# Performance work log

Hardware: AMD Instinct MI355X
Metric: run time of the kernel (lower is better)

## Reference

```python
import jax, jax.numpy as jnp
import numpy as np

B, D, E = 8, 256, 2048
H, DK, DV = 8, 32, 32
LN_EPS = 1e-6
MASK_FILL = -1e9


def setup_inputs() -> dict:
    key = jax.random.key(0)
    ks = jax.random.split(key, 6)
    scale = 1.0 / np.sqrt(D)
    x = jax.random.normal(ks[0], (B, D, E), dtype=jnp.float32)
    mask = jax.random.randint(ks[1], (B, E, E), 0, 2).astype(bool)
    w_qs = jax.random.normal(ks[2], (D, H * DK), dtype=jnp.float32) * scale
    w_ks = jax.random.normal(ks[3], (D, H * DK), dtype=jnp.float32) * scale
    w_vs = jax.random.normal(ks[4], (D, H * DV), dtype=jnp.float32) * scale
    w_fc = jax.random.normal(ks[5], (H * DV, D), dtype=jnp.float32) * scale
    ln_gamma = jnp.ones((D,), dtype=jnp.float32)
    ln_beta = jnp.zeros((D,), dtype=jnp.float32)
    return {"x": x, "mask": mask, "w_qs": w_qs, "w_ks": w_ks,
            "w_vs": w_vs, "w_fc": w_fc, "ln_gamma": ln_gamma, "ln_beta": ln_beta}


def reference(x, mask, w_qs, w_ks, w_vs, w_fc, ln_gamma, ln_beta):
    # x: [B, D, E] -> s: [B, E, D]  (edges as sequence, features as d_model)
    s = jnp.transpose(x, (0, 2, 1))
    residual = s
    # LayerNorm applied to queries only (as in the original MultiHeadAttention)
    mu = jnp.mean(s, axis=-1, keepdims=True)
    var = jnp.mean((s - mu) ** 2, axis=-1, keepdims=True)
    q_in = (s - mu) * jax.lax.rsqrt(var + LN_EPS) * ln_gamma + ln_beta
    # projections -> [B, H, E, dk/dv]
    q = (q_in @ w_qs).reshape(B, E, H, DK).transpose(0, 2, 1, 3)
    k = (s @ w_ks).reshape(B, E, H, DK).transpose(0, 2, 1, 3)
    v = (s @ w_vs).reshape(B, E, H, DV).transpose(0, 2, 1, 3)
    temperature = jnp.sqrt(jnp.asarray(DK, dtype=q.dtype))
    scores = jnp.einsum('bhqd,bhkd->bhqk', q / temperature, k)
    scores = jnp.where(mask[:, None, :, :], scores, MASK_FILL)
    attn = jax.nn.softmax(scores, axis=-1)  # [B, H, E, E]
    out = jnp.einsum('bhqk,bhkd->bhqd', attn, v)
    out = out.transpose(0, 2, 1, 3).reshape(B, E, H * DV)
    out = out @ w_fc + residual  # dropout is identity in eval mode
    x_out = jnp.transpose(out, (0, 2, 1))  # back to [B, D, E]
    # attention-per-edge diagnostic (no gradient in original: attn.detach())
    attn_d = jax.lax.stop_gradient(attn)
    m = mask[:, None, :, :].astype(attn.dtype)  # [B, 1, E, E]
    attn_per_edge = jnp.sum(attn_d * m, axis=(1, 2)) / jnp.sum(m, axis=(1, 2))
    return (x_out, attn, attn_per_edge)
```

## Files before the change

### kernel.cpp

```cpp
#include <hip/hip_runtime.h>
#include <hip/hip_fp16.h>
#include <math.h>

#define TB 8
#define TD 256
#define TE 2048
#define TH 8

typedef _Float16 h8 __attribute__((ext_vector_type(8)));
typedef float    f4 __attribute__((ext_vector_type(4)));

static __device__ __forceinline__ unsigned int packh2(float a, float b){
  __half2 h = __floats2half2_rn(a, b);
  return __builtin_bit_cast(unsigned int, h);
}

__global__ __launch_bounds__(256) void k_pack(const unsigned int* __restrict__ mraw,
                       unsigned int* __restrict__ packed, float* __restrict__ num){
  __shared__ int oks;
  const int t = threadIdx.x;
  if(t == 0) oks = 1;
  __syncthreads();
  int ok = 1;
  for(int i=t; i<4096; i+=256) if(mraw[i] > 1u) ok = 0;
  if(!ok) atomicAnd(&oks, 0);
  __syncthreads();
  const int isInt = oks;

  const int row = blockIdx.x*4 + (t >> 6);
  const int w = t & 63;
  const size_t base = (size_t)row*TE + (size_t)w*32;
  unsigned int bits = 0;
  if(isInt){
    const unsigned int* p = mraw + base;
    #pragma unroll
    for(int j=0;j<32;j++) bits |= (p[j] & 1u) << j;
  } else {
    const unsigned char* p = (const unsigned char*)mraw + base;
    #pragma unroll
    for(int j=0;j<32;j++) bits |= (unsigned int)(p[j] != 0) << j;
  }
  packed[(size_t)row*64 + w] = bits;
  if(blockIdx.x < 64) num[blockIdx.x*256 + t] = 0.f;
}

__global__ __launch_bounds__(256) void k_denom(const unsigned int* __restrict__ packed,
                        float* __restrict__ denom){
  const int b = blockIdx.z;
  const int k = blockIdx.x*256 + threadIdx.x;
  const int q0 = blockIdx.y*64;
  const unsigned int* p = packed + ((size_t)b*TE + q0)*64 + (k >> 5);
  const unsigned sh = k & 31;
  int cnt = 0;
  #pragma unroll 8
  for(int q=0;q<64;q++) cnt += (p[(size_t)q*64] >> sh) & 1u;
  atomicAdd(&denom[b*TE + k], (float)cnt);
}

__global__ __launch_bounds__(256) void k_wpack(
    const float* __restrict__ wqs, const float* __restrict__ wks,
    const float* __restrict__ wvs, const float* __restrict__ wfc,
    _Float16* __restrict__ qkvT, _Float16* __restrict__ fcT){
  const int n = blockIdx.x;
  const int k = threadIdx.x;
  if(n < 256)      qkvT[(size_t)n*256 + k] = (_Float16)wqs[(size_t)k*256 + n];
  else if(n < 512) qkvT[(size_t)n*256 + k] = (_Float16)wks[(size_t)k*256 + (n-256)];
  else if(n < 768) qkvT[(size_t)n*256 + k] = (_Float16)wvs[(size_t)k*256 + (n-512)];
  else             fcT[(size_t)(n-768)*256 + k] = (_Float16)wfc[(size_t)k*256 + (n-768)];
}

__global__ __launch_bounds__(256) void k_qkv(
    const float* __restrict__ x, const _Float16* __restrict__ qkvT,
    const float* __restrict__ gamma, const float* __restrict__ beta,
    _Float16* __restrict__ qh, _Float16* __restrict__ kh, _Float16* __restrict__ vt){
  __shared__ float xs[16][260];
  __shared__ __align__(16) _Float16 xh[16][264];
  __shared__ __align__(16) _Float16 qn[16][264];
  __shared__ float mu_s[16], rs_s[16];
  const int t = threadIdx.x;
  const int b = blockIdx.y;
  const int e0 = blockIdx.x*16;

  for(int i=t;i<16*256;i+=256){
    int el = i & 15, dd = i >> 4;
    xs[el][dd] = x[((size_t)(b*TD + dd))*TE + e0 + el];
  }
  __syncthreads();
  {
    int row = t >> 4, j = t & 15;
    float s1=0.f, s2=0.f;
    #pragma unroll
    for(int i=0;i<16;i++){ float v = xs[row][j*16+i]; s1 += v; s2 += v*v; }
    #pragma unroll
    for(int off=1; off<16; off<<=1){ s1 += __shfl_xor(s1, off); s2 += __shfl_xor(s2, off); }
    if(j==0){
      float m = s1 * (1.f/256.f);
      float var = s2 * (1.f/256.f) - m*m;
      mu_s[row] = m;
      rs_s[row] = rsqrtf(var + 1e-6f);
    }
  }
  __syncthreads();
  for(int i=t;i<16*256;i+=256){
    int r = i >> 8, dd = i & 255;
    float xv = xs[r][dd];
    xh[r][dd] = (_Float16)xv;
    qn[r][dd] = (_Float16)((xv - mu_s[r]) * rs_s[r] * gamma[dd] + beta[dd]);
  }
  __syncthreads();

  const int w = t >> 6, l = t & 63, g = l >> 4, c = l & 15;
  const f4 f4z = {0.f,0.f,0.f,0.f};
  const float sclq = 0.17677669529663687f * 1.44269504088896f;
  h8 af[8];

  #pragma unroll
  for(int kk=0;kk<8;kk++) af[kk] = *(const h8*)&qn[c][kk*32 + g*8];
  #pragma unroll
  for(int i=0;i<4;i++){
    const int n0 = (4*w+i)*16;
    f4 acc = f4z;
    #pragma unroll
    for(int kk=0;kk<8;kk++){
      h8 bf = *(const h8*)(qkvT + (size_t)(n0 + c)*256 + kk*32 + g*8);
      acc = __builtin_amdgcn_mfma_f32_16x16x32_f16(bf, af[kk], acc, 0, 0, 0);
    }
    const int d0 = n0 + 4*g, hh = d0 >> 5, d2 = d0 & 31;
    uint2 ov;
    ov.x = packh2(acc[0]*sclq, acc[1]*sclq);
    ov.y = packh2(acc[2]*sclq, acc[3]*sclq);
    *(uint2*)&qh[((size_t)(b*TH+hh)*TE + e0 + c)*32 + d2] = ov;
  }
  #pragma unroll
  for(int kk=0;kk<8;kk++) af[kk] = *(const h8*)&xh[c][kk*32 + g*8];
  #pragma unroll
  for(int i=0;i<4;i++){
    const int n0 = (4*w+i)*16;
    f4 acc = f4z;
    #pragma unroll
    for(int kk=0;kk<8;kk++){
      h8 bf = *(const h8*)(qkvT + (size_t)(256 + n0 + c)*256 + kk*32 + g*8);
      acc = __builtin_amdgcn_mfma_f32_16x16x32_f16(bf, af[kk], acc, 0, 0, 0);
    }
    const int d0 = n0 + 4*g, hh = d0 >> 5, d2 = d0 & 31;
    uint2 ov;
    ov.x = packh2(acc[0], acc[1]);
    ov.y = packh2(acc[2], acc[3]);
    *(uint2*)&kh[((size_t)(b*TH+hh)*TE + e0 + c)*32 + d2] = ov;
  }
  const int jj = (e0 >> 4) & 1;
  const int p = c & 3, a = c >> 2;
  #pragma unroll
  for(int i=0;i<4;i++){
    const int n0 = (4*w+i)*16;
    f4 acc = f4z;
    #pragma unroll
    for(int kk=0;kk<8;kk++){
      h8 bf = *(const h8*)(qkvT + (size_t)(512 + n0 + c)*256 + kk*32 + g*8);
      acc = __builtin_amdgcn_mfma_f32_16x16x32_f16(bf, af[kk], acc, 0, 0, 0);
    }
    f4 n_, fv;
    #pragma unroll
    for(int r=0;r<4;r++){
      float o = __shfl_xor(acc[r^1], 1);
      n_[r] = ((p^r)&1) ? o : acc[r];
    }
    #pragma unroll
    for(int r=0;r<4;r++){
      float o = __shfl_xor(n_[r^2], 2);
      fv[r] = ((p^r)&2) ? o : n_[r];
    }
    const int d = n0 + 4*g + p;
    uint2 ov;
    ov.x = packh2(fv[0], fv[1]);
    ov.y = packh2(fv[2], fv[3]);
    *(uint2*)&vt[((size_t)(b*TH + (d>>5))*32 + (d&31))*TE + (e0 & ~31) + 8*a + 4*jj] = ov;
  }
}

__global__ __launch_bounds__(256) void k_attn(
    const _Float16* __restrict__ qh, const _Float16* __restrict__ kh, const _Float16* __restrict__ vt,
    const unsigned int* __restrict__ packed,
    float* __restrict__ attn, _Float16* __restrict__ owh, float* __restrict__ num){
  __shared__ __align__(16) unsigned int mb[64][66];
  __shared__ float num_s[TE];
  __shared__ __align__(16) f4 S4[4][272];

  const int t = threadIdx.x;
  int bid = blockIdx.x;
  bid = (bid & 7) * 256 + (bid >> 3);
  const int qt = bid & 31;
  const int bhid = bid >> 5;
  const int h = bhid & 7, b = bhid >> 3;
  const size_t bh = (size_t)bhid * TE;
  const _Float16* Qg = qh + bh*32;
  const _Float16* Kg = kh + bh*32;
  const _Float16* Vg = vt + bh*32;
  const int q0 = qt*64;

  const int wid = t >> 6, l = t & 63, g = l >> 4, c = l & 15;
  const int qr = wid*16 + c;
  const f4 f4z = {0.f, 0.f, 0.f, 0.f};

  for(int i=t;i<TE;i+=256) num_s[i] = 0.f;
  for(int i=t;i<64*64;i+=256){
    int r = i >> 6, w = i & 63;
    mb[r][w] = packed[((size_t)b*TE + q0 + r)*64 + w];
  }
  __syncthreads();

  const h8 qf = *(const h8*)(Qg + (size_t)(q0 + qr)*32 + g*8);

  float ll = 0.f;
  for(int kt=0; kt<32; ++kt){
    h8 kf[4];
    #pragma unroll
    for(int j=0;j<4;j++) kf[j] = *(const h8*)(Kg + (size_t)(kt*64 + j*16 + c)*32 + g*8);
    f4 s[4];
    #pragma unroll
    for(int j=0;j<4;j++) s[j] = __builtin_amdgcn_mfma_f32_16x16x32_f16(kf[j], qf, f4z, 0, 0, 0);
    const uint2 mw2 = *(const uint2*)&mb[qr][2*kt];
    #pragma unroll
    for(int j=0;j<4;j++){
      const unsigned mw = (j>>1) ? mw2.y : mw2.x;
      #pragma unroll
      for(int r=0;r<4;r++){
        float sv = ((mw >> ((j&1)*16 + 4*g + r)) & 1u) ? s[j][r] : -1e9f;
        ll += exp2f(sv);
      }
    }
  }
  ll += __shfl_xor(ll, 16);
  ll += __shfl_xor(ll, 32);
  const float rl = 1.f / ll;

  f4 oacc[2] = {f4z, f4z};
  f4* Sw = S4[wid];
  float* abase = attn + (bh + q0 + wid*16)*TE;
  for(int kt=0; kt<32; ++kt){
    h8 kf[4];
    #pragma unroll
    for(int j=0;j<4;j++) kf[j] = *(const h8*)(Kg + (size_t)(kt*64 + j*16 + c)*32 + g*8);
    f4 s[4];
    #pragma unroll
    for(int j=0;j<4;j++) s[j] = __builtin_amdgcn_mfma_f32_16x16x32_f16(kf[j], qf, f4z, 0, 0, 0);
    const uint2 mw2 = *(const uint2*)&mb[qr][2*kt];
    unsigned int pk[4][2];
    #pragma unroll
    for(int j=0;j<4;j++){
      const unsigned mw = (j>>1) ? mw2.y : mw2.x;
      f4 p;
      #pragma unroll
      for(int r=0;r<4;r++){
        float sv = ((mw >> ((j&1)*16 + 4*g + r)) & 1u) ? s[j][r] : -1e9f;
        p[r] = exp2f(sv) * rl;
      }
      Sw[c*17 + 4*j + g] = p;
      pk[j][0] = packh2(p[0], p[1]);
      pk[j][1] = packh2(p[2], p[3]);
    }
    #pragma unroll
    for(int kc=0;kc<2;kc++){
      uint4 pu = {pk[2*kc][0], pk[2*kc][1], pk[2*kc+1][0], pk[2*kc+1][1]};
      h8 pf = __builtin_bit_cast(h8, pu);
      #pragma unroll
      for(int du=0;du<2;du++){
        h8 vf = *(const h8*)(Vg + (size_t)(du*16 + c)*TE + kt*64 + kc*32 + g*8);
        oacc[du] = __builtin_amdgcn_mfma_f32_16x16x32_f16(vf, pf, oacc[du], 0, 0, 0);
      }
    }
    f4 v[4];
    #pragma unroll
    for(int u=0;u<4;u++) v[u] = Sw[(u*4+g)*17 + c];
    #pragma unroll
    for(int u=0;u<4;u++)
      __builtin_nontemporal_store(v[u], (f4*)(abase + (size_t)(u*4+g)*TE + kt*64 + c*4));
    f4 a = v[0] + v[1] + v[2] + v[3];
    #pragma unroll
    for(int q=0;q<4;q++){ a[q] += __shfl_xor(a[q], 16); a[q] += __shfl_xor(a[q], 32); }
    if(l < 16){
      float* np = &num_s[kt*64 + c*4];
      atomicAdd(np+0, a[0]); atomicAdd(np+1, a[1]);
      atomicAdd(np+2, a[2]); atomicAdd(np+3, a[3]);
    }
  }

  #pragma unroll
  for(int du=0;du<2;du++){
    uint2 ov;
    ov.x = packh2(oacc[du][0], oacc[du][1]);
    ov.y = packh2(oacc[du][2], oacc[du][3]);
    *(uint2*)&owh[((size_t)b*TE + q0 + qr)*256 + h*32 + du*16 + 4*g] = ov;
  }
  __syncthreads();
  for(int i=t;i<TE;i+=256) atomicAdd(&num[(size_t)b*TE + i], num_s[i]);
}

__global__ __launch_bounds__(256) void k_fc(
    const _Float16* __restrict__ owh, const _Float16* __restrict__ fcT,
    const float* __restrict__ x, float* __restrict__ xout){
  __shared__ float xt[16][260];
  const int t = threadIdx.x;
  const int b = blockIdx.y;
  const int e0 = blockIdx.x * 16;
  for(int i=t;i<4096;i+=256){
    int el = i & 15, dd = i >> 4;
    xt[el][dd] = x[((size_t)(b*TD + dd))*TE + e0 + el];
  }
  const int w = t >> 6, l = t & 63, g = l >> 4, c = l & 15;
  h8 af[8];
  #pragma unroll
  for(int kk=0;kk<8;kk++)
    af[kk] = *(const h8*)(owh + ((size_t)b*TE + e0 + c)*256 + kk*32 + g*8);
  f4 accs[4];
  #pragma unroll
  for(int i=0;i<4;i++){
    const int n0 = w*64 + i*16;
    f4 acc = {0.f,0.f,0.f,0.f};
    #pragma unroll
    for(int kk=0;kk<8;kk++){
      h8 bf = *(const h8*)(fcT + (size_t)(n0 + c)*256 + kk*32 + g*8);
      acc = __builtin_amdgcn_mfma_f32_16x16x32_f16(bf, af[kk], acc, 0, 0, 0);
    }
    accs[i] = acc;
  }
  __syncthreads();
  #pragma unroll
  for(int i=0;i<4;i++){
    const int n0 = w*64 + i*16 + 4*g;
    #pragma unroll
    for(int r=0;r<4;r++) xt[c][n0+r] += accs[i][r];
  }
  __syncthreads();
  for(int i=t;i<4096;i+=256){
    int el = i & 15, dd = i >> 4;
    xout[((size_t)(b*TD + dd))*TE + e0 + el] = xt[el][dd];
  }
}

__global__ void k_edge(const float* __restrict__ num, const float* __restrict__ denom,
                       float* __restrict__ pe){
  int idx = blockIdx.x*256 + threadIdx.x;
  pe[idx] = num[idx] / (8.f * denom[idx]);
}

extern "C" void kernel_launch(void* const* d_in, const int* in_sizes, int n_in,
                              void* d_out, int out_size, void* d_ws, size_t ws_size,
                              hipStream_t stream){
  const float* x   = (const float*)d_in[0];
  const unsigned int* mraw = (const unsigned int*)d_in[1];
  const float* wqs = (const float*)d_in[2];
  const float* wks = (const float*)d_in[3];
  const float* wvs = (const float*)d_in[4];
  const float* wfc = (const float*)d_in[5];
  const float* gamma = (const float*)d_in[6];
  const float* beta  = (const float*)d_in[7];

  float* xout = (float*)d_out;
  float* attn = xout + (size_t)TB*TD*TE;
  float* pe   = attn + (size_t)TB*TH*TE*TE;

  const size_t SZ = (size_t)TB*TH*TE*32;
  _Float16* qhp = (_Float16*)((char*)d_ws + 256);
  _Float16* khp = qhp + SZ;
  _Float16* vtp = khp + SZ;
  _Float16* owh = vtp + SZ;
  unsigned int* packed = (unsigned int*)(owh + SZ);
  float* num   = (float*)(packed + (size_t)TB*TE*64);
  float* denom = num + (size_t)TB*TE;
  _Float16* qkvT = (_Float16*)(denom + (size_t)TB*TE);
  _Float16* fcT  = qkvT + 768*256;

  hipMemsetAsync(denom, 0, (size_t)TB*TE*sizeof(float), stream);
  k_wpack<<<1024, 256, 0, stream>>>(wqs, wks, wvs, wfc, qkvT, fcT);
  k_pack<<<TB*TE/4, 256, 0, stream>>>(mraw, packed, num);
  k_denom<<<dim3(TE/256, TE/64, TB), 256, 0, stream>>>(packed, denom);
  k_qkv<<<dim3(TE/16, TB), 256, 0, stream>>>(x, qkvT, gamma, beta, qhp, khp, vtp);
  k_attn<<<TB*TH*TE/64, 256, 0, stream>>>(qhp, khp, vtp, packed, attn, owh, num);
  k_fc<<<dim3(TE/16, TB), 256, 0, stream>>>(owh, fcT, x, xout);
  k_edge<<<TB*TE/256, 256, 0, stream>>>(num, denom, pe);
}
```

Before: 403.8 us.

## Fuse mask column counts into coalesced ballot-based mask packing; drop k_denom

```diff
diff --git a/kernel.cpp b/kernel.cpp
--- a/kernel.cpp
+++ b/kernel.cpp
@@ -16,8 +16,10 @@
 }
 
 __global__ __launch_bounds__(256) void k_pack(const unsigned int* __restrict__ mraw,
-                       unsigned int* __restrict__ packed, float* __restrict__ num){
+                       unsigned int* __restrict__ packed, float* __restrict__ denom,
+                       float* __restrict__ num){
   __shared__ int oks;
+  __shared__ unsigned int ps[32][66];
   const int t = threadIdx.x;
   if(t == 0) oks = 1;
   __syncthreads();
@@ -27,34 +29,34 @@
   __syncthreads();
   const int isInt = oks;
 
-  const int row = blockIdx.x*4 + (t >> 6);
-  const int w = t & 63;
-  const size_t base = (size_t)row*TE + (size_t)w*32;
-  unsigned int bits = 0;
-  if(isInt){
-    const unsigned int* p = mraw + base;
-    #pragma unroll
-    for(int j=0;j<32;j++) bits |= (p[j] & 1u) << j;
-  } else {
-    const unsigned char* p = (const unsigned char*)mraw + base;
-    #pragma unroll
-    for(int j=0;j<32;j++) bits |= (unsigned int)(p[j] != 0) << j;
-  }
-  packed[(size_t)row*64 + w] = bits;
+  const int b = blockIdx.x >> 6;
+  const int q0 = (blockIdx.x & 63) * 32;
+  const int w = t >> 6, l = t & 63;
+  int cnt[8] = {0,0,0,0,0,0,0,0};
+  for(int r=0; r<32; ++r){
+    const size_t rb = ((size_t)b*TE + q0 + r) * (size_t)TE;
+    #pragma unroll
+    for(int s=0; s<8; ++s){
+      const int k = s*256 + t;
+      int bit;
+      if(isInt) bit = (int)(mraw[rb + k] & 1u);
+      else      bit = (((const unsigned char*)mraw)[rb + k] != 0) ? 1 : 0;
+      cnt[s] += bit;
+      unsigned long long bal = __ballot(bit);
+      if(l == 0){
+        ps[r][s*8 + w*2]     = (unsigned int)bal;
+        ps[r][s*8 + w*2 + 1] = (unsigned int)(bal >> 32);
+      }
+    }
+  }
+  __syncthreads();
+  for(int i=t; i<32*64; i+=256){
+    int r = i >> 6, wd = i & 63;
+    packed[((size_t)b*TE + q0 + r)*64 + wd] = ps[r][wd];
+  }
+  #pragma unroll
+  for(int s=0; s<8; ++s) atomicAdd(&denom[b*TE + s*256 + t], (float)cnt[s]);
   if(blockIdx.x < 64) num[blockIdx.x*256 + t] = 0.f;
-}
-
-__global__ __launch_bounds__(256) void k_denom(const unsigned int* __restrict__ packed,
-                        float* __restrict__ denom){
-  const int b = blockIdx.z;
-  const int k = blockIdx.x*256 + threadIdx.x;
-  const int q0 = blockIdx.y*64;
-  const unsigned int* p = packed + ((size_t)b*TE + q0)*64 + (k >> 5);
-  const unsigned sh = k & 31;
-  int cnt = 0;
-  #pragma unroll 8
-  for(int q=0;q<64;q++) cnt += (p[(size_t)q*64] >> sh) & 1u;
-  atomicAdd(&denom[b*TE + k], (float)cnt);
 }
 
 __global__ __launch_bounds__(256) void k_wpack(
@@ -183,7 +185,6 @@
     const unsigned int* __restrict__ packed,
     float* __restrict__ attn, _Float16* __restrict__ owh, float* __restrict__ num){
   __shared__ __align__(16) unsigned int mb[64][66];
-  __shared__ float num_s[TE];
   __shared__ __align__(16) f4 S4[4][272];
 
   const int t = threadIdx.x;
@@ -202,7 +203,6 @@
   const int qr = wid*16 + c;
   const f4 f4z = {0.f, 0.f, 0.f, 0.f};
 
-  for(int i=t;i<TE;i+=256) num_s[i] = 0.f;
   for(int i=t;i<64*64;i+=256){
     int r = i >> 6, w = i & 63;
     mb[r][w] = packed[((size_t)b*TE + q0 + r)*64 + w];
@@ -211,7 +211,7 @@
 
   const h8 qf = *(const h8*)(Qg + (size_t)(q0 + qr)*32 + g*8);
 
-  float ll = 0.f;
+  float ll4[4] = {0.f, 0.f, 0.f, 0.f};
   for(int kt=0; kt<32; ++kt){
     h8 kf[4];
     #pragma unroll
@@ -226,17 +226,19 @@
       #pragma unroll
       for(int r=0;r<4;r++){
         float sv = ((mw >> ((j&1)*16 + 4*g + r)) & 1u) ? s[j][r] : -1e9f;
-        ll += exp2f(sv);
+        ll4[j] += exp2f(sv);
       }
     }
   }
+  float ll = (ll4[0] + ll4[1]) + (ll4[2] + ll4[3]);
   ll += __shfl_xor(ll, 16);
   ll += __shfl_xor(ll, 32);
-  const float rl = 1.f / ll;
+  const float lr = -__log2f(ll);
 
   f4 oacc[2] = {f4z, f4z};
   f4* Sw = S4[wid];
   float* abase = attn + (bh + q0 + wid*16)*TE;
+  float* nbase = num + (size_t)b*TE;
   for(int kt=0; kt<32; ++kt){
     h8 kf[4];
     #pragma unroll
@@ -253,7 +255,7 @@
       #pragma unroll
       for(int r=0;r<4;r++){
         float sv = ((mw >> ((j&1)*16 + 4*g + r)) & 1u) ? s[j][r] : -1e9f;
-        p[r] = exp2f(sv) * rl;
+        p[r] = exp2f(sv + lr);
       }
       Sw[c*17 + 4*j + g] = p;
       pk[j][0] = packh2(p[0], p[1]);
@@ -279,7 +281,7 @@
     #pragma unroll
     for(int q=0;q<4;q++){ a[q] += __shfl_xor(a[q], 16); a[q] += __shfl_xor(a[q], 32); }
     if(l < 16){
-      float* np = &num_s[kt*64 + c*4];
+      float* np = nbase + kt*64 + c*4;
       atomicAdd(np+0, a[0]); atomicAdd(np+1, a[1]);
       atomicAdd(np+2, a[2]); atomicAdd(np+3, a[3]);
     }
@@ -292,8 +294,6 @@
     ov.y = packh2(oacc[du][2], oacc[du][3]);
     *(uint2*)&owh[((size_t)b*TE + q0 + qr)*256 + h*32 + du*16 + 4*g] = ov;
   }
-  __syncthreads();
-  for(int i=t;i<TE;i+=256) atomicAdd(&num[(size_t)b*TE + i], num_s[i]);
 }
 
 __global__ __launch_bounds__(256) void k_fc(
@@ -373,8 +373,7 @@
 
   hipMemsetAsync(denom, 0, (size_t)TB*TE*sizeof(float), stream);
   k_wpack<<<1024, 256, 0, stream>>>(wqs, wks, wvs, wfc, qkvT, fcT);
-  k_pack<<<TB*TE/4, 256, 0, stream>>>(mraw, packed, num);
-  k_denom<<<dim3(TE/256, TE/64, TB), 256, 0, stream>>>(packed, denom);
+  k_pack<<<TB*TE/32, 256, 0, stream>>>(mraw, packed, denom, num);
   k_qkv<<<dim3(TE/16, TB), 256, 0, stream>>>(x, qkvT, gamma, beta, qhp, khp, vtp);
   k_attn<<<TB*TH*TE/64, 256, 0, stream>>>(qhp, khp, vtp, packed, attn, owh, num);
   k_fc<<<dim3(TE/16, TB), 256, 0, stream>>>(owh, fcT, x, xout);
```

After: 633.4 us. +56.9%, slower.

## Split attn staging into half-tiles with XOR-swizzled LDS, fuse edge kernel into fc

Applied to the files above, without the earlier changes.

```diff
diff --git a/kernel.cpp b/kernel.cpp
--- a/kernel.cpp
+++ b/kernel.cpp
@@ -178,13 +178,13 @@
   }
 }
 
-__global__ __launch_bounds__(256) void k_attn(
+__global__ __launch_bounds__(256, 4) void k_attn(
     const _Float16* __restrict__ qh, const _Float16* __restrict__ kh, const _Float16* __restrict__ vt,
     const unsigned int* __restrict__ packed,
     float* __restrict__ attn, _Float16* __restrict__ owh, float* __restrict__ num){
   __shared__ __align__(16) unsigned int mb[64][66];
   __shared__ float num_s[TE];
-  __shared__ __align__(16) f4 S4[4][272];
+  __shared__ __align__(16) f4 S4h[4][16][9];
 
   const int t = threadIdx.x;
   int bid = blockIdx.x;
@@ -235,8 +235,10 @@
   const float rl = 1.f / ll;
 
   f4 oacc[2] = {f4z, f4z};
-  f4* Sw = S4[wid];
+  f4 (*Sw)[9] = S4h[wid];
   float* abase = attn + (bh + q0 + wid*16)*TE;
+  const int rr = l >> 3;
+  const int ch = l & 7;
   for(int kt=0; kt<32; ++kt){
     h8 kf[4];
     #pragma unroll
@@ -245,43 +247,47 @@
     #pragma unroll
     for(int j=0;j<4;j++) s[j] = __builtin_amdgcn_mfma_f32_16x16x32_f16(kf[j], qf, f4z, 0, 0, 0);
     const uint2 mw2 = *(const uint2*)&mb[qr][2*kt];
-    unsigned int pk[4][2];
-    #pragma unroll
-    for(int j=0;j<4;j++){
-      const unsigned mw = (j>>1) ? mw2.y : mw2.x;
-      f4 p;
+    #pragma unroll
+    for(int h2=0; h2<2; ++h2){
+      const unsigned mw = h2 ? mw2.y : mw2.x;
+      unsigned int pk0[2][2];
       #pragma unroll
-      for(int r=0;r<4;r++){
-        float sv = ((mw >> ((j&1)*16 + 4*g + r)) & 1u) ? s[j][r] : -1e9f;
-        p[r] = exp2f(sv) * rl;
-      }
-      Sw[c*17 + 4*j + g] = p;
-      pk[j][0] = packh2(p[0], p[1]);
-      pk[j][1] = packh2(p[2], p[3]);
-    }
-    #pragma unroll
-    for(int kc=0;kc<2;kc++){
-      uint4 pu = {pk[2*kc][0], pk[2*kc][1], pk[2*kc+1][0], pk[2*kc+1][1]};
-      h8 pf = __builtin_bit_cast(h8, pu);
+      for(int j2=0;j2<2;j2++){
+        f4 p;
+        #pragma unroll
+        for(int r=0;r<4;r++){
+          float sv = ((mw >> (j2*16 + 4*g + r)) & 1u) ? s[2*h2+j2][r] : -1e9f;
+          p[r] = exp2f(sv) * rl;
+        }
+        Sw[c][((j2<<2)|g) ^ (c&7)] = p;
+        pk0[j2][0] = packh2(p[0], p[1]);
+        pk0[j2][1] = packh2(p[2], p[3]);
+      }
+      {
+        uint4 pu = {pk0[0][0], pk0[0][1], pk0[1][0], pk0[1][1]};
+        h8 pf = __builtin_bit_cast(h8, pu);
+        #pragma unroll
+        for(int du=0;du<2;du++){
+          h8 vf = *(const h8*)(Vg + (size_t)(du*16 + c)*TE + kt*64 + h2*32 + g*8);
+          oacc[du] = __builtin_amdgcn_mfma_f32_16x16x32_f16(vf, pf, oacc[du], 0, 0, 0);
+        }
+      }
+      f4 v0 = Sw[rr][ch ^ rr];
+      f4 v1 = Sw[8 + rr][ch ^ rr];
+      __builtin_nontemporal_store(v0, (f4*)(abase + (size_t)rr*TE     + kt*64 + h2*32 + ch*4));
+      __builtin_nontemporal_store(v1, (f4*)(abase + (size_t)(8+rr)*TE + kt*64 + h2*32 + ch*4));
+      f4 a = v0 + v1;
       #pragma unroll
-      for(int du=0;du<2;du++){
-        h8 vf = *(const h8*)(Vg + (size_t)(du*16 + c)*TE + kt*64 + kc*32 + g*8);
-        oacc[du] = __builtin_amdgcn_mfma_f32_16x16x32_f16(vf, pf, oacc[du], 0, 0, 0);
-      }
-    }
-    f4 v[4];
-    #pragma unroll
-    for(int u=0;u<4;u++) v[u] = Sw[(u*4+g)*17 + c];
-    #pragma unroll
-    for(int u=0;u<4;u++)
-      __builtin_nontemporal_store(v[u], (f4*)(abase + (size_t)(u*4+g)*TE + kt*64 + c*4));
-    f4 a = v[0] + v[1] + v[2] + v[3];
-    #pragma unroll
-    for(int q=0;q<4;q++){ a[q] += __shfl_xor(a[q], 16); a[q] += __shfl_xor(a[q], 32); }
-    if(l < 16){
-      float* np = &num_s[kt*64 + c*4];
-      atomicAdd(np+0, a[0]); atomicAdd(np+1, a[1]);
-      atomicAdd(np+2, a[2]); atomicAdd(np+3, a[3]);
+      for(int q=0;q<4;q++){
+        a[q] += __shfl_xor(a[q], 8);
+        a[q] += __shfl_xor(a[q], 16);
+        a[q] += __shfl_xor(a[q], 32);
+      }
+      if(l < 8){
+        float* np = &num_s[kt*64 + h2*32 + l*4];
+        atomicAdd(np+0, a[0]); atomicAdd(np+1, a[1]);
+        atomicAdd(np+2, a[2]); atomicAdd(np+3, a[3]);
+      }
     }
   }
 
@@ -298,11 +304,16 @@
 
 __global__ __launch_bounds__(256) void k_fc(
     const _Float16* __restrict__ owh, const _Float16* __restrict__ fcT,
-    const float* __restrict__ x, float* __restrict__ xout){
+    const float* __restrict__ x, float* __restrict__ xout,
+    const float* __restrict__ num, const float* __restrict__ denom, float* __restrict__ pe){
   __shared__ float xt[16][260];
   const int t = threadIdx.x;
   const int b = blockIdx.y;
   const int e0 = blockIdx.x * 16;
+  if(blockIdx.x < 8){
+    int idx = (b*8 + blockIdx.x)*256 + t;
+    pe[idx] = num[idx] / (8.f * denom[idx]);
+  }
   for(int i=t;i<4096;i+=256){
     int el = i & 15, dd = i >> 4;
     xt[el][dd] = x[((size_t)(b*TD + dd))*TE + e0 + el];
@@ -336,12 +347,6 @@
     int el = i & 15, dd = i >> 4;
     xout[((size_t)(b*TD + dd))*TE + e0 + el] = xt[el][dd];
   }
-}
-
-__global__ void k_edge(const float* __restrict__ num, const float* __restrict__ denom,
-                       float* __restrict__ pe){
-  int idx = blockIdx.x*256 + threadIdx.x;
-  pe[idx] = num[idx] / (8.f * denom[idx]);
 }
 
 extern "C" void kernel_launch(void* const* d_in, const int* in_sizes, int n_in,
@@ -377,6 +382,5 @@
   k_denom<<<dim3(TE/256, TE/64, TB), 256, 0, stream>>>(packed, denom);
   k_qkv<<<dim3(TE/16, TB), 256, 0, stream>>>(x, qkvT, gamma, beta, qhp, khp, vtp);
   k_attn<<<TB*TH*TE/64, 256, 0, stream>>>(qhp, khp, vtp, packed, attn, owh, num);
-  k_fc<<<dim3(TE/16, TB), 256, 0, stream>>>(owh, fcT, x, xout);
-  k_edge<<<TB*TE/256, 256, 0, stream>>>(num, denom, pe);
-}
+  k_fc<<<dim3(TE/16, TB), 256, 0, stream>>>(owh, fcT, x, xout, num, denom, pe);
+}
```

Measured after the change: 410.8 us. Within noise of the previous version (+1.7%).
